# Kernel optimization log

Measured on AMD Instinct MI355X. Metric: run time of the kernel, lower is better.

Reference implementation:

```python
import jax, jax.numpy as jnp
import numpy as np

DIM = 192
HEADS = 6
HIDDEN = 384  # int(DIM * 2.0)


def _ln(x, w, b):
    # WithBias LayerNorm over channel dim (torch normalizes last dim of b,(hw),c)
    mu = jnp.mean(x, axis=1, keepdims=True)
    var = jnp.var(x, axis=1, keepdims=True)
    return (x - mu) / jnp.sqrt(var + 1e-5) * w[None, :, None, None] + b[None, :, None, None]


def _conv1x1(x, w):  # w: [O, I, 1, 1]
    return jnp.einsum('bihw,oi->bohw', x, w[:, :, 0, 0])


def _dwconv3(x, w):  # depthwise 3x3, w: [C, 1, 3, 3]
    return jax.lax.conv_general_dilated(
        x, w, window_strides=(1, 1), padding=((1, 1), (1, 1)),
        feature_group_count=x.shape[1],
        dimension_numbers=('NCHW', 'OIHW', 'NCHW'))


def _l2norm(x):  # F.normalize along last axis
    n = jnp.sqrt(jnp.sum(x * x, axis=-1, keepdims=True))
    return x / jnp.maximum(n, 1e-12)


def setup_inputs() -> dict:
    key = jax.random.key(0)
    ks = jax.random.split(key, 16)
    s = 0.02
    d = {}
    d['x'] = jax.random.normal(ks[0], (2, DIM, 128, 128), dtype=jnp.float32)
    d['k_v'] = jax.random.normal(ks[1], (2, 256), dtype=jnp.float32)
    d['ln1_w'] = jnp.ones((DIM,), jnp.float32)
    d['ln1_b'] = jnp.zeros((DIM,), jnp.float32)
    d['temp'] = jnp.ones((HEADS, 1, 1), jnp.float32)
    d['w_kR'] = jax.random.normal(ks[2], (DIM * 3 // 4, 192), jnp.float32) * s
    d['w_kI'] = jax.random.normal(ks[3], (DIM // 4, 64), jnp.float32) * s
    d['w_qR'] = jax.random.normal(ks[4], (DIM, DIM * 3 // 4, 1, 1), jnp.float32) * s
    d['w_qdw'] = jax.random.normal(ks[5], (DIM, 1, 3, 3), jnp.float32) * s
    d['w_kvI'] = jax.random.normal(ks[6], (DIM * 2, DIM // 4, 1, 1), jnp.float32) * s
    d['w_kvdw'] = jax.random.normal(ks[7], (DIM * 2, 1, 3, 3), jnp.float32) * s
    d['w_po'] = jax.random.normal(ks[8], (DIM, DIM, 1, 1), jnp.float32) * s
    d['ln2_w'] = jnp.ones((DIM,), jnp.float32)
    d['ln2_b'] = jnp.zeros((DIM,), jnp.float32)
    d['w_ffk'] = jax.random.normal(ks[9], (DIM, 256), jnp.float32) * s
    d['w_pin'] = jax.random.normal(ks[10], (HIDDEN * 2, DIM, 1, 1), jnp.float32) * s
    d['w_dw'] = jax.random.normal(ks[11], (HIDDEN * 2, 1, 3, 3), jnp.float32) * s
    d['w_pout'] = jax.random.normal(ks[12], (DIM, HIDDEN, 1, 1), jnp.float32) * s
    return d


def reference(x, k_v, ln1_w, ln1_b, temp, w_kR, w_kI, w_qR, w_qdw, w_kvI, w_kvdw,
              w_po, ln2_w, ln2_b, w_ffk, w_pin, w_dw, w_pout):
    b, c, h, w = x.shape
    c3 = c * 3 // 4
    # ---- Rttention on norm1(x) ----
    xn = _ln(x, ln1_w, ln1_b)
    kvr = (k_v[:, :192] @ w_kR.T)[:, :, None, None]   # [b, 3c/4, 1, 1]
    kvi = (k_v[:, 192:] @ w_kI.T)[:, :, None, None]   # [b, c/4, 1, 1]
    x_r = xn[:, :c3] * kvr + xn[:, :c3]
    x_i = xn[:, c3:] * kvi + xn[:, c3:]
    q = _dwconv3(_conv1x1(x_r, w_qR), w_qdw)          # [b, c, h, w]
    kv = _dwconv3(_conv1x1(x_i, w_kvI), w_kvdw)       # [b, 2c, h, w]
    k, v = jnp.split(kv, 2, axis=1)
    rh = lambda t: t.reshape(b, HEADS, c // HEADS, h * w)
    q = _l2norm(rh(q))
    k = _l2norm(rh(k))
    v = rh(v)
    # channel-wise attention: [b, head, c_h, c_h]
    attn = jax.nn.softmax(jnp.einsum('bhcd,bhed->bhce', q, k) * temp[None], axis=-1)
    out = jnp.einsum('bhce,bhed->bhcd', attn, v).reshape(b, c, h, w)
    x = x + _conv1x1(out, w_po)
    # ---- GDFN FeedForward on norm2(x) ----
    xn2 = _ln(x, ln2_w, ln2_b)
    kvf = (k_v @ w_ffk.T)[:, :, None, None]           # [b, c, 1, 1]
    y = xn2 * kvf + xn2
    y = _dwconv3(_conv1x1(y, w_pin), w_dw)            # [b, 2*hidden, h, w]
    y1, y2 = jnp.split(y, 2, axis=1)
    y = jax.nn.gelu(y1, approximate=False) * y2
    x = x + _conv1x1(y, w_pout)
    return (x, k_v)
```

## Files before the change

### kernel.cpp

```cpp
#include <hip/hip_runtime.h>
#include <math.h>

#define HW 16384
#define CDIM 192
#define C3 144
#define C4 48
#define NB 2
#define NPX 32768
#define HEADS 6

typedef unsigned short u16;
typedef unsigned int u32;
typedef __attribute__((ext_vector_type(8))) short bf16x8;
typedef __attribute__((ext_vector_type(4))) float f32x4;

__device__ __forceinline__ float bf2f(u16 u) {
    return __uint_as_float(((unsigned int)u) << 16);
}
__device__ __forceinline__ u16 f2bf(float f) {
    unsigned int x = __float_as_uint(f);
    unsigned int r = x + 0x7fffu + ((x >> 16) & 1u);
    return (u16)(r >> 16);
}

static inline float* wsf(void* ws, size_t off) { return (float*)((char*)ws + off); }
static inline u16* wsh(void* ws, size_t off) { return (u16*)((char*)ws + off); }

__global__ void k_setup(const float* __restrict__ kvv, const float* __restrict__ wkR,
                        const float* __restrict__ wkI, const float* __restrict__ wffk,
                        const float* __restrict__ wqR, const float* __restrict__ wkvI,
                        const float* __restrict__ wpo, const float* __restrict__ wpin,
                        const float* __restrict__ wpout,
                        const float* __restrict__ ln2w, const float* __restrict__ ln2b,
                        u16* __restrict__ wb, float* __restrict__ sm,
                        float* __restrict__ A2, float* __restrict__ B2,
                        float* __restrict__ tail) {
    int t = blockIdx.x * 256 + threadIdx.x;
    if (t < 313344) {
        float v;
        if (t < 30720) {
            int o = t / 160, i = t % 160;
            v = (i < 144) ? wqR[o * 144 + i] : 0.f;
        } else if (t < 55296) {
            int r = t - 30720; int o = r / 64, i = r % 64;
            v = (i < 48) ? wkvI[o * 48 + i] : 0.f;
        } else if (t < 92160) {
            v = wpo[t - 55296];
        } else if (t < 239616) {
            v = wpin[t - 92160];
        } else {
            v = wpout[t - 239616];
        }
        wb[t] = f2bf(v);
    } else if (t < 314112) {
        int r = t - 313344;
        if (r < 288) {
            int b = r / 144, o = r % 144;
            const float* v = kvv + b * 256;
            const float* w = wkR + o * 192;
            float s = 0.f;
            for (int j = 0; j < 192; j++) s += v[j] * w[j];
            sm[r] = s + 1.0f;
        } else if (r < 384) {
            int r2 = r - 288;
            int b = r2 / 48, o = r2 % 48;
            const float* v = kvv + b * 256 + 192;
            const float* w = wkI + o * 64;
            float s = 0.f;
            for (int j = 0; j < 64; j++) s += v[j] * w[j];
            sm[288 + r2] = s + 1.0f;
        } else {
            int r2 = r - 384;
            int b = r2 / 192, o = r2 % 192;
            const float* v = kvv + b * 256;
            const float* w = wffk + o * 256;
            float s = 0.f;
            for (int j = 0; j < 256; j++) s += v[j] * w[j];
            float sc = s + 1.0f;
            sm[384 + r2] = sc;
            A2[r2] = ln2w[o] * sc;
            B2[r2] = ln2b[o] * sc;
        }
    } else if (t < 314624) {
        int r = t - 314112;
        tail[r] = kvv[r];
    }
}

__global__ __launch_bounds__(256) void k_ln1(
    const float* __restrict__ xin,
    const float* __restrict__ lnw, const float* __restrict__ lnb,
    const float* __restrict__ sca, const float* __restrict__ scb,
    u16* __restrict__ outA, u16* __restrict__ outB) {
    __shared__ float red[2][16][16][4];
    __shared__ float mu_s[16][4], rstd_s[16][4];
    int t = threadIdx.x;
    int px4 = t & 15, cg = t >> 4;
    int base = blockIdx.x * 64;
    int b = base >> 14;
    int p = (base & 16383) + px4 * 4;
    float vals[12][4];
    float s[4] = {0.f, 0.f, 0.f, 0.f}, s2[4] = {0.f, 0.f, 0.f, 0.f};
#pragma unroll
    for (int j = 0; j < 12; j++) {
        int c = cg * 12 + j;
        size_t off = ((size_t)(b * CDIM + c)) * HW + p;
        float4 f = *(const float4*)(xin + off);
        float v[4] = {f.x, f.y, f.z, f.w};
#pragma unroll
        for (int q = 0; q < 4; q++) {
            vals[j][q] = v[q]; s[q] += v[q]; s2[q] += v[q] * v[q];
        }
    }
#pragma unroll
    for (int q = 0; q < 4; q++) { red[0][cg][px4][q] = s[q]; red[1][cg][px4][q] = s2[q]; }
    __syncthreads();
    if (t < 16) {
        float S[4] = {0.f, 0.f, 0.f, 0.f}, S2[4] = {0.f, 0.f, 0.f, 0.f};
        for (int g2 = 0; g2 < 16; g2++)
#pragma unroll
            for (int q = 0; q < 4; q++) { S[q] += red[0][g2][t][q]; S2[q] += red[1][g2][t][q]; }
#pragma unroll
        for (int q = 0; q < 4; q++) {
            float mu = S[q] * (1.0f / CDIM);
            float var = S2[q] * (1.0f / CDIM) - mu * mu;
            mu_s[t][q] = mu;
            rstd_s[t][q] = rsqrtf(var + 1e-5f);
        }
    }
    __syncthreads();
    float mu[4], rs[4];
#pragma unroll
    for (int q = 0; q < 4; q++) { mu[q] = mu_s[px4][q]; rs[q] = rstd_s[px4][q]; }
    float Ac[12], Bc[12];
#pragma unroll
    for (int j = 0; j < 12; j++) {
        int c = cg * 12 + j;
        float sc = (c < C3) ? sca[b * C3 + c] : scb[b * C4 + (c - C3)];
        Ac[j] = lnw[c] * sc;
        Bc[j] = lnb[c] * sc;
    }
    int isR = (cg < 12);
    size_t row0 = (size_t)b * HW + p;
    u16* basep = isR ? (outA + row0 * 160 + cg * 12)
                     : (outB + row0 * 64 + (cg * 12 - 144));
    int rowlen = isR ? 160 : 64;
#pragma unroll
    for (int q = 0; q < 4; q++) {
        u16 tmp[12];
#pragma unroll
        for (int j = 0; j < 12; j++)
            tmp[j] = f2bf((vals[j][q] - mu[q]) * rs[q] * Ac[j] + Bc[j]);
        u16* op = basep + q * rowlen;
        ushort4 o0 = {tmp[0], tmp[1], tmp[2], tmp[3]};
        ushort4 o1 = {tmp[4], tmp[5], tmp[6], tmp[7]};
        ushort4 o2 = {tmp[8], tmp[9], tmp[10], tmp[11]};
        *(ushort4*)(op) = o0;
        *(ushort4*)(op + 4) = o1;
        *(ushort4*)(op + 8) = o2;
    }
    if (cg == 0) {
        int4 z = {0, 0, 0, 0};
#pragma unroll
        for (int q = 0; q < 4; q++) {
            u16* pr = outA + (row0 + q) * 160 + 144;
            *(int4*)(pr) = z; *(int4*)(pr + 8) = z;
            u16* pi = outB + (row0 + q) * 64 + 48;
            *(int4*)(pi) = z; *(int4*)(pi + 8) = z;
        }
    }
}

template <int NCH, int MODE>
__global__ __launch_bounds__(256) void k_gemm_t(
    const u16* __restrict__ X, const u16* __restrict__ Wb,
    const void* __restrict__ resid, void* __restrict__ outp, int CO) {
    constexpr int CIP = NCH * 32;
    __shared__ __align__(16) u16 Xs[128 * 40];
    __shared__ __align__(16) u16 Wsh[64 * 40];
    const int tid = threadIdx.x;
    const int n0 = blockIdx.x * 128;
    const int m0 = blockIdx.y * 64;
    const int b = blockIdx.z;
    const int wave = tid >> 6, lane = tid & 63;
    const int quad = lane >> 4, l16 = lane & 15;
    const int spx = tid >> 1, sh = tid & 1;
    const int swr = tid >> 2, swc = tid & 3;
    const u16* xsrc = X + ((size_t)b * HW + n0 + spx) * CIP + sh * 16;
    const u16* wsrc = Wb + (size_t)(m0 + swr) * CIP + swc * 8;
    int4 xr0 = *(const int4*)(xsrc);
    int4 xr1 = *(const int4*)(xsrc + 8);
    int4 wr0 = *(const int4*)(wsrc);
    f32x4 acc[4][2] = {};
#pragma unroll
    for (int ch = 0; ch < NCH; ch++) {
        if (ch) __syncthreads();
        *(int4*)&Xs[spx * 40 + sh * 16] = xr0;
        *(int4*)&Xs[spx * 40 + sh * 16 + 8] = xr1;
        *(int4*)&Wsh[swr * 40 + swc * 8] = wr0;
        if (ch + 1 < NCH) {
            xr0 = *(const int4*)(xsrc + (ch + 1) * 32);
            xr1 = *(const int4*)(xsrc + (ch + 1) * 32 + 8);
            wr0 = *(const int4*)(wsrc + (ch + 1) * 32);
        }
        __syncthreads();
        bf16x8 af[4];
#pragma unroll
        for (int mi = 0; mi < 4; mi++)
            af[mi] = *(const bf16x8*)&Wsh[(mi * 16 + l16) * 40 + quad * 8];
        bf16x8 bf0 = *(const bf16x8*)&Xs[(wave * 32 + l16) * 40 + quad * 8];
        bf16x8 bf1 = *(const bf16x8*)&Xs[(wave * 32 + 16 + l16) * 40 + quad * 8];
#pragma unroll
        for (int mi = 0; mi < 4; mi++) {
            acc[mi][0] = __builtin_amdgcn_mfma_f32_16x16x32_bf16(af[mi], bf0, acc[mi][0], 0, 0, 0);
            acc[mi][1] = __builtin_amdgcn_mfma_f32_16x16x32_bf16(af[mi], bf1, acc[mi][1], 0, 0, 0);
        }
    }
#pragma unroll
    for (int mi = 0; mi < 4; mi++) {
#pragma unroll
        for (int ni = 0; ni < 2; ni++) {
            int c0 = m0 + mi * 16 + quad * 4;
            int px = n0 + wave * 32 + ni * 16 + l16;
            if (MODE == 0) {
                u16* ob = (u16*)outp + ((size_t)b * CO + c0) * HW + px;
#pragma unroll
                for (int rr = 0; rr < 4; rr++) ob[(size_t)rr * HW] = f2bf(acc[mi][ni][rr]);
            } else {
                const float* rp = (const float*)resid + ((size_t)b * 192 + c0) * HW + px;
                ushort4 o;
                o.x = f2bf(acc[mi][ni][0] + rp[0]);
                o.y = f2bf(acc[mi][ni][1] + rp[(size_t)HW]);
                o.z = f2bf(acc[mi][ni][2] + rp[(size_t)2 * HW]);
                o.w = f2bf(acc[mi][ni][3] + rp[(size_t)3 * HW]);
                *(ushort4*)((u16*)outp + ((size_t)b * HW + px) * 192 + c0) = o;
            }
        }
    }
}

__global__ __launch_bounds__(256) void k_gemm_s(
    const u16* __restrict__ X, const u16* __restrict__ Wb,
    const u16* __restrict__ residT, float* __restrict__ outp) {
    constexpr int NCH = 12;
    constexpr int CIP = NCH * 32;
    __shared__ __align__(16) u16 Ws[64 * 32];
    __shared__ __align__(16) u16 Xs[32 * 130];
    const int tid = threadIdx.x;
    const int n0 = blockIdx.x * 128;
    const int m0 = blockIdx.y * 64;
    const int b = blockIdx.z;
    const u16* Xb = X + (size_t)b * 384 * HW + n0;
    const int wave = tid >> 6, lane = tid & 63;
    const int quad = lane >> 4, l16 = lane & 15;
    const int smr = tid >> 2, sk4 = tid & 3;
    const int skr = tid >> 3, sc0 = (tid & 7) * 16;
    f32x4 acc[4][2] = {};
    for (int ch = 0; ch < NCH; ch++) {
        const int k0 = ch * 32;
        if (ch) __syncthreads();
        {
            const int4 wv = *(const int4*)(Wb + (size_t)(m0 + smr) * CIP + k0 + sk4 * 8);
            *(int4*)&Ws[(smr << 5) + (((sk4 ^ (smr & 3)) & 3) << 3)] = wv;
        }
        {
            const u16* xc = Xb + (size_t)(k0 + skr) * HW + sc0;
            int4 r0 = *(const int4*)xc;
            int4 r1 = *(const int4*)(xc + 8);
            u32* dst = (u32*)&Xs[skr * 130 + sc0];
#pragma unroll
            for (int i = 0; i < 4; i++) dst[i] = ((const u32*)&r0)[i];
#pragma unroll
            for (int i = 0; i < 4; i++) dst[4 + i] = ((const u32*)&r1)[i];
        }
        __syncthreads();
        bf16x8 af[4];
#pragma unroll
        for (int mi = 0; mi < 4; mi++) {
            int row = mi * 16 + l16;
            af[mi] = *(const bf16x8*)&Ws[(row << 5) + ((quad ^ (row & 3)) << 3)];
        }
#pragma unroll
        for (int ni = 0; ni < 2; ni++) {
            int n = wave * 32 + ni * 16 + l16;
            bf16x8 bfr;
#pragma unroll
            for (int j = 0; j < 8; j++) bfr[j] = (short)Xs[(quad * 8 + j) * 130 + n];
#pragma unroll
            for (int mi = 0; mi < 4; mi++)
                acc[mi][ni] = __builtin_amdgcn_mfma_f32_16x16x32_bf16(af[mi], bfr, acc[mi][ni], 0, 0, 0);
        }
    }
#pragma unroll
    for (int mi = 0; mi < 4; mi++) {
#pragma unroll
        for (int ni = 0; ni < 2; ni++) {
            int c0 = m0 + mi * 16 + quad * 4;
            int px = n0 + wave * 32 + ni * 16 + l16;
            ushort4 rv = *(const ushort4*)(residT + ((size_t)b * HW + px) * 192 + c0);
            float* ob = outp + ((size_t)b * 192 + c0) * HW + px;
            ob[0] = acc[mi][ni][0] + bf2f(rv.x);
            ob[(size_t)HW] = acc[mi][ni][1] + bf2f(rv.y);
            ob[(size_t)2 * HW] = acc[mi][ni][2] + bf2f(rv.z);
            ob[(size_t)3 * HW] = acc[mi][ni][3] + bf2f(rv.w);
        }
    }
}

__global__ __launch_bounds__(256) void k_dw2(const u16* __restrict__ X,
                                             const float* __restrict__ Wd,
                                             u16* __restrict__ out, int C, int sqCh,
                                             float* __restrict__ sqp) {
    __shared__ float In[34 * 132];
    __shared__ float red[4];
    int bc = blockIdx.x >> 2, rt = blockIdx.x & 3;
    int b = bc / C, ch = bc % C;
    const u16* xb = X + (size_t)bc * HW;
    int t = threadIdx.x;
    int c0 = (t & 7) * 16;
    for (int r = t >> 3; r < 34; r += 32) {
        int y = rt * 32 - 1 + r;
        float* dst = &In[r * 132 + 1 + c0];
        if ((unsigned)y < 128u) {
            const u16* src = xb + y * 128 + c0;
            int4 r0 = *(const int4*)src;
            int4 r1 = *(const int4*)(src + 8);
            const u16* p0 = (const u16*)&r0;
            const u16* p1 = (const u16*)&r1;
#pragma unroll
            for (int i = 0; i < 8; i++) dst[i] = bf2f(p0[i]);
#pragma unroll
            for (int i = 0; i < 8; i++) dst[8 + i] = bf2f(p1[i]);
        } else {
#pragma unroll
            for (int i = 0; i < 16; i++) dst[i] = 0.f;
        }
    }
    if (t < 34) { In[t * 132] = 0.f; In[t * 132 + 129] = 0.f; }
    __syncthreads();
    const float* w = Wd + ch * 9;
    float w00 = w[0], w01 = w[1], w02 = w[2], w10 = w[3], w11 = w[4],
          w12 = w[5], w20 = w[6], w21 = w[7], w22 = w[8];
    int x = t & 127, rg = t >> 7;
    int base = rg * 16;
    float A2 = 0.f, A1 = 0.f, B1 = 0.f, ssq = 0.f;
    u16* ob = out + (size_t)bc * HW + (rt * 32 + base) * 128 + x;
#pragma unroll
    for (int r = 0; r < 18; r++) {
        const float* row = &In[(base + r) * 132 + x];
        float v0 = row[0], v1 = row[1], v2 = row[2];
        float h0 = w00 * v0 + w01 * v1 + w02 * v2;
        float h1 = w10 * v0 + w11 * v1 + w12 * v2;
        float h2 = w20 * v0 + w21 * v1 + w22 * v2;
        if (r >= 2) {
            float val = A2 + B1 + h2;
            ob[(size_t)(r - 2) * 128] = f2bf(val);
            ssq += val * val;
        }
        A2 = A1; A1 = h0; B1 = h1;
    }
    if (ch < sqCh) {
        for (int o = 32; o > 0; o >>= 1) ssq += __shfl_down(ssq, o, 64);
        int wid = t >> 6, lane = t & 63;
        if (lane == 0) red[wid] = ssq;
        __syncthreads();
        if (t == 0) sqp[((b * 192 + ch) << 2) | rt] = red[0] + red[1] + red[2] + red[3];
    }
}

__global__ __launch_bounds__(256) void k_dw_gelu2(const u16* __restrict__ G0,
                                                  const float* __restrict__ Wd,
                                                  u16* __restrict__ out) {
    __shared__ float In[2 * 34 * 132];
    int bc = blockIdx.x >> 2, rt = blockIdx.x & 3;
    int b = bc / 384, j = bc % 384;
    int t = threadIdx.x;
    int c0 = (t & 7) * 16;
    for (int pl = 0; pl < 2; pl++) {
        const u16* xb = G0 + ((size_t)b * 768 + pl * 384 + j) * HW;
        float* pla = &In[pl * 34 * 132];
        for (int r = t >> 3; r < 34; r += 32) {
            int y = rt * 32 - 1 + r;
            float* dst = &pla[r * 132 + 1 + c0];
            if ((unsigned)y < 128u) {
                const u16* src = xb + y * 128 + c0;
                int4 r0 = *(const int4*)src;
                int4 r1 = *(const int4*)(src + 8);
                const u16* p0 = (const u16*)&r0;
                const u16* p1 = (const u16*)&r1;
#pragma unroll
                for (int i = 0; i < 8; i++) dst[i] = bf2f(p0[i]);
#pragma unroll
                for (int i = 0; i < 8; i++) dst[8 + i] = bf2f(p1[i]);
            } else {
#pragma unroll
                for (int i = 0; i < 16; i++) dst[i] = 0.f;
            }
        }
        if (t < 34) { pla[t * 132] = 0.f; pla[t * 132 + 129] = 0.f; }
    }
    __syncthreads();
    const float* w1 = Wd + j * 9;
    const float* w2 = Wd + (384 + j) * 9;
    float a00 = w1[0], a01 = w1[1], a02 = w1[2], a10 = w1[3], a11 = w1[4],
          a12 = w1[5], a20 = w1[6], a21 = w1[7], a22 = w1[8];
    float b00 = w2[0], b01 = w2[1], b02 = w2[2], b10 = w2[3], b11 = w2[4],
          b12 = w2[5], b20 = w2[6], b21 = w2[7], b22 = w2[8];
    int x = t & 127, rg = t >> 7;
    int base = rg * 16;
    float A2a = 0.f, A1a = 0.f, B1a = 0.f;
    float A2b = 0.f, A1b = 0.f, B1b = 0.f;
    u16* ob = out + ((size_t)b * 384 + j) * HW + (rt * 32 + base) * 128 + x;
#pragma unroll
    for (int r = 0; r < 18; r++) {
        const float* r1p = &In[(base + r) * 132 + x];
        const float* r2p = r1p + 34 * 132;
        float u0 = r1p[0], u1 = r1p[1], u2 = r1p[2];
        float v0 = r2p[0], v1 = r2p[1], v2 = r2p[2];
        float h0a = a00 * u0 + a01 * u1 + a02 * u2;
        float h1a = a10 * u0 + a11 * u1 + a12 * u2;
        float h2a = a20 * u0 + a21 * u1 + a22 * u2;
        float h0b = b00 * v0 + b01 * v1 + b02 * v2;
        float h1b = b10 * v0 + b11 * v1 + b12 * v2;
        float h2b = b20 * v0 + b21 * v1 + b22 * v2;
        if (r >= 2) {
            float s1 = A2a + B1a + h2a;
            float s2 = A2b + B1b + h2b;
            float g = 0.5f * s1 * (1.0f + erff(s1 * 0.70710678118654752f));
            ob[(size_t)(r - 2) * 128] = f2bf(g * s2);
        }
        A2a = A1a; A1a = h0a; B1a = h1a;
        A2b = A1b; A1b = h0b; B1b = h1b;
    }
}

__global__ __launch_bounds__(256) void k_qk(const u16* __restrict__ qb_,
                                            const u16* __restrict__ kb_,
                                            float* __restrict__ Spart) {
    int bh = blockIdx.x >> 6, ds = blockIdx.x & 63;
    int b = bh / HEADS, h = bh % HEADS;
    int tid = threadIdx.x;
    int wave = tid >> 6, lane = tid & 63;
    int quad = lane >> 4, l16 = lane & 15;
    int tm = wave >> 1, tn = wave & 1;
    const u16* qrow = qb_ + ((size_t)(b * 192 + h * 32 + tm * 16 + l16)) * HW + ds * 256 + quad * 8;
    const u16* krow = kb_ + ((size_t)(b * 384 + h * 32 + tn * 16 + l16)) * HW + ds * 256 + quad * 8;
    f32x4 acc = {};
    bf16x8 qa[3], ka[3];
    auto ld = [&](int s, int cc) {
        qa[s] = *(const bf16x8*)(qrow + cc * 32);
        ka[s] = *(const bf16x8*)(krow + cc * 32);
    };
    ld(0, 0); ld(1, 1);
#pragma unroll
    for (int ch = 0; ch < 8; ch++) {
        if (ch + 2 < 8) ld((ch + 2) % 3, ch + 2);
        acc = __builtin_amdgcn_mfma_f32_16x16x32_bf16(qa[ch % 3], ka[ch % 3], acc, 0, 0, 0);
    }
    float* Sb = Spart + ((size_t)ds * 12 + bh) * 1024;
#pragma unroll
    for (int r = 0; r < 4; r++)
        Sb[(tm * 16 + quad * 4 + r) * 32 + tn * 16 + l16] = acc[r];
}

__global__ void k_softmax(const float* __restrict__ Spart, const float* __restrict__ sqqp,
                          const float* __restrict__ sqkp, const float* __restrict__ temp,
                          u16* __restrict__ attnb) {
    int row = blockIdx.x;
    int bh = row >> 5, c2 = row & 31;
    int b = bh / HEADS, h = bh % HEADS;
    int e = threadIdx.x;
    float l = -1e30f;
    if (e < 32) {
        float s = 0.f;
        for (int d = 0; d < 64; d++) s += Spart[((size_t)d * 12 + bh) * 1024 + c2 * 32 + e];
        const float* qp = sqqp + (b * 192 + h * 32 + c2) * 4;
        const float* kp = sqkp + (b * 192 + h * 32 + e) * 4;
        float nq = qp[0] + qp[1] + qp[2] + qp[3];
        float nk = kp[0] + kp[1] + kp[2] + kp[3];
        float invq = 1.0f / fmaxf(sqrtf(nq), 1e-12f);
        float invk = 1.0f / fmaxf(sqrtf(nk), 1e-12f);
        l = s * invq * invk * temp[h];
    }
    float m = l;
    for (int o = 32; o > 0; o >>= 1) m = fmaxf(m, __shfl_xor(m, o, 64));
    float ev = (e < 32) ? expf(l - m) : 0.f;
    float ssum = ev;
    for (int o = 32; o > 0; o >>= 1) ssum += __shfl_xor(ssum, o, 64);
    if (e < 32) attnb[bh * 1024 + c2 * 32 + e] = f2bf(ev / ssum);
}

__global__ __launch_bounds__(256) void k_av(const u16* __restrict__ attnb,
                                            const u16* __restrict__ kvb,
                                            u16* __restrict__ out) {
    __shared__ __align__(16) u16 Vs[32 * 130];
    int bh = blockIdx.x >> 7;
    int pt = blockIdx.x & 127;
    int b = bh / HEADS, h = bh % HEADS;
    int p0 = pt * 128;
    int t = threadIdx.x;
    {
        int e = t >> 3, c0 = (t & 7) * 16;
        const u16* src = kvb + ((size_t)(b * 384 + 192 + h * 32 + e)) * HW + p0 + c0;
        int4 r0 = *(const int4*)src;
        int4 r1 = *(const int4*)(src + 8);
        u32* dst = (u32*)&Vs[e * 130 + c0];
#pragma unroll
        for (int i = 0; i < 4; i++) dst[i] = ((const u32*)&r0)[i];
#pragma unroll
        for (int i = 0; i < 4; i++) dst[4 + i] = ((const u32*)&r1)[i];
    }
    __syncthreads();
    int wave = t >> 6, lane = t & 63;
    int quad = lane >> 4, l16 = lane & 15;
    f32x4 acc[2][2] = {};
    bf16x8 af[2];
#pragma unroll
    for (int tm = 0; tm < 2; tm++)
        af[tm] = *(const bf16x8*)(attnb + bh * 1024 + (tm * 16 + l16) * 32 + quad * 8);
#pragma unroll
    for (int nt = 0; nt < 2; nt++) {
        int n = wave * 32 + nt * 16 + l16;
        bf16x8 bfr;
#pragma unroll
        for (int j = 0; j < 8; j++) bfr[j] = (short)Vs[(quad * 8 + j) * 130 + n];
#pragma unroll
        for (int tm = 0; tm < 2; tm++)
            acc[tm][nt] = __builtin_amdgcn_mfma_f32_16x16x32_bf16(af[tm], bfr, acc[tm][nt], 0, 0, 0);
    }
#pragma unroll
    for (int tm = 0; tm < 2; tm++)
#pragma unroll
        for (int nt = 0; nt < 2; nt++) {
            int c0 = h * 32 + tm * 16 + quad * 4;
            int px = p0 + wave * 32 + nt * 16 + l16;
            ushort4 o;
            o.x = f2bf(acc[tm][nt][0]);
            o.y = f2bf(acc[tm][nt][1]);
            o.z = f2bf(acc[tm][nt][2]);
            o.w = f2bf(acc[tm][nt][3]);
            *(ushort4*)(out + ((size_t)b * HW + px) * 192 + c0) = o;
        }
}

__global__ __launch_bounds__(256) void k_ln2t(
    const u16* __restrict__ xin, const float* __restrict__ A2,
    const float* __restrict__ B2, u16* __restrict__ outp) {
    int t = threadIdx.x;
    int pxg = blockIdx.x * 64 + (t >> 2);
    int l2 = t & 3;
    int b = pxg >> 14;
    const u16* src = xin + (size_t)pxg * 192 + l2 * 48;
    float v[48];
    float s = 0.f, s2 = 0.f;
#pragma unroll
    for (int i = 0; i < 6; i++) {
        int4 r0 = *(const int4*)(src + i * 8);
        const u16* pp = (const u16*)&r0;
#pragma unroll
        for (int k = 0; k < 8; k++) {
            float f = bf2f(pp[k]);
            v[i * 8 + k] = f; s += f; s2 += f * f;
        }
    }
    s += __shfl_xor(s, 1, 64);  s += __shfl_xor(s, 2, 64);
    s2 += __shfl_xor(s2, 1, 64); s2 += __shfl_xor(s2, 2, 64);
    float mu = s * (1.0f / CDIM);
    float rstd = rsqrtf(s2 * (1.0f / CDIM) - mu * mu + 1e-5f);
    const float* Ap = A2 + b * 192 + l2 * 48;
    const float* Bp = B2 + b * 192 + l2 * 48;
    u16* dst = outp + (size_t)pxg * 192 + l2 * 48;
#pragma unroll
    for (int i = 0; i < 12; i++) {
        float4 a = *(const float4*)(Ap + i * 4);
        float4 bb = *(const float4*)(Bp + i * 4);
        ushort4 o;
        o.x = f2bf((v[i * 4 + 0] - mu) * rstd * a.x + bb.x);
        o.y = f2bf((v[i * 4 + 1] - mu) * rstd * a.y + bb.y);
        o.z = f2bf((v[i * 4 + 2] - mu) * rstd * a.z + bb.z);
        o.w = f2bf((v[i * 4 + 3] - mu) * rstd * a.w + bb.w);
        *(ushort4*)(dst + i * 4) = o;
    }
}

extern "C" void kernel_launch(void* const* d_in, const int* in_sizes, int n_in,
                              void* d_out, int out_size, void* d_ws, size_t ws_size,
                              hipStream_t stream) {
    const float* x     = (const float*)d_in[0];
    const float* k_v   = (const float*)d_in[1];
    const float* ln1w  = (const float*)d_in[2];
    const float* ln1b  = (const float*)d_in[3];
    const float* temp  = (const float*)d_in[4];
    const float* w_kR  = (const float*)d_in[5];
    const float* w_kI  = (const float*)d_in[6];
    const float* w_qR  = (const float*)d_in[7];
    const float* w_qdw = (const float*)d_in[8];
    const float* w_kvI = (const float*)d_in[9];
    const float* w_kvdw= (const float*)d_in[10];
    const float* w_po  = (const float*)d_in[11];
    const float* ln2w  = (const float*)d_in[12];
    const float* ln2b  = (const float*)d_in[13];
    const float* w_ffk = (const float*)d_in[14];
    const float* w_pin = (const float*)d_in[15];
    const float* w_dw  = (const float*)d_in[16];
    const float* w_pout= (const float*)d_in[17];
    float* out = (float*)d_out;

    const size_t MiB = 1048576ULL;
    u16*   q0b     = wsh(d_ws, 0);
    u16*   attnoutb= wsh(d_ws, 0);
    u16*   y0b     = wsh(d_ws, 0);
    u16*   kv0b    = wsh(d_ws, 12 * MiB);
    u16*   ybufb   = wsh(d_ws, 12 * MiB);
    u16*   x1b     = wsh(d_ws, 36 * MiB);
    u16*   qbuf_b  = wsh(d_ws, 48 * MiB);
    u16*   kvbuf_b = wsh(d_ws, 60 * MiB);
    u16*   xrb     = wsh(d_ws, 84 * MiB);
    u16*   xib     = wsh(d_ws, 94 * MiB);
    u16*   g0b     = wsh(d_ws, 98 * MiB);
    u16*   wb      = wsh(d_ws, 146 * MiB);
    float* sm      = wsf(d_ws, 147 * MiB);
    float* Spart   = wsf(d_ws, 0);
    u16* wq   = wb;
    u16* wkv  = wb + 30720;
    u16* wpo  = wb + 55296;
    u16* wpin = wb + 92160;
    u16* wpout= wb + 239616;
    float* kvr  = sm;
    float* kvi  = sm + 288;
    float* sqqp = sm + 768;
    float* sqkp = sm + 2304;
    u16*   attnb= (u16*)(sm + 3840);
    float* A2c  = sm + 10240;
    float* B2c  = sm + 10624;

    k_setup<<<1229, 256, 0, stream>>>(k_v, w_kR, w_kI, w_ffk, w_qR, w_kvI, w_po,
                                      w_pin, w_pout, ln2w, ln2b, wb, sm, A2c, B2c,
                                      out + (size_t)NB * CDIM * HW);
    k_ln1<<<NPX / 64, 256, 0, stream>>>(x, ln1w, ln1b, kvr, kvi, xrb, xib);
    k_gemm_t<5, 0><<<dim3(128, 3, 2), 256, 0, stream>>>(xrb, wq, nullptr, q0b, 192);
    k_gemm_t<2, 0><<<dim3(128, 6, 2), 256, 0, stream>>>(xib, wkv, nullptr, kv0b, 384);
    k_dw2<<<NB * 192 * 4, 256, 0, stream>>>(q0b, w_qdw, qbuf_b, 192, 192, sqqp);
    k_dw2<<<NB * 384 * 4, 256, 0, stream>>>(kv0b, w_kvdw, kvbuf_b, 384, 192, sqkp);
    k_qk<<<12 * 64, 256, 0, stream>>>(qbuf_b, kvbuf_b, Spart);
    k_softmax<<<384, 64, 0, stream>>>(Spart, sqqp, sqkp, temp, attnb);
    k_av<<<12 * 128, 256, 0, stream>>>(attnb, kvbuf_b, attnoutb);
    k_gemm_t<6, 1><<<dim3(128, 3, 2), 256, 0, stream>>>(attnoutb, wpo, x, x1b, 192);
    k_ln2t<<<NPX / 64, 256, 0, stream>>>(x1b, A2c, B2c, y0b);
    k_gemm_t<6, 0><<<dim3(128, 12, 2), 256, 0, stream>>>(y0b, wpin, nullptr, g0b, 768);
    k_dw_gelu2<<<NB * 384 * 4, 256, 0, stream>>>(g0b, w_dw, ybufb);
    k_gemm_s<<<dim3(128, 3, 2), 256, 0, stream>>>(ybufb, wpout, x1b, out);
}
```

Baseline: 262.4 us.

## Fuse output projection GEMM with residual and LayerNorm2; vectorize depthwise smem staging

Adds a new GEMM kernel for the attention output projection in which each block computes all 192 output channels for 64 pixels. This lets it add the residual and apply LayerNorm2 with the k_v scale in registers, writing both x1 and the normalized FFN input, so the separate LN2 pass and its reread of x1 go away. The depthwise-conv kernels pad shared-memory rows to 136 floats so bf16 inputs can be staged with float4 stores, and the setup dot-product loops get unroll pragmas. In exchange, the fused kernel holds 12 accumulators plus a 48-float array per thread, which may raise register pressure, and it reads the residual with a strided per-channel pattern.

```diff
diff --git a/kernel.cpp b/kernel.cpp
--- a/kernel.cpp
+++ b/kernel.cpp
@@ -59,6 +59,7 @@
             const float* v = kvv + b * 256;
             const float* w = wkR + o * 192;
             float s = 0.f;
+#pragma unroll 8
             for (int j = 0; j < 192; j++) s += v[j] * w[j];
             sm[r] = s + 1.0f;
         } else if (r < 384) {
@@ -67,6 +68,7 @@
             const float* v = kvv + b * 256 + 192;
             const float* w = wkI + o * 64;
             float s = 0.f;
+#pragma unroll 8
             for (int j = 0; j < 64; j++) s += v[j] * w[j];
             sm[288 + r2] = s + 1.0f;
         } else {
@@ -75,6 +77,7 @@
             const float* v = kvv + b * 256;
             const float* w = wffk + o * 256;
             float s = 0.f;
+#pragma unroll 8
             for (int j = 0; j < 256; j++) s += v[j] * w[j];
             float sc = s + 1.0f;
             sm[384 + r2] = sc;
@@ -236,6 +239,83 @@
                 *(ushort4*)((u16*)outp + ((size_t)b * HW + px) * 192 + c0) = o;
             }
         }
+    }
+}
+
+__global__ __launch_bounds__(256) void k_gemm_po(
+    const u16* __restrict__ X, const u16* __restrict__ Wb,
+    const float* __restrict__ resid, const float* __restrict__ A2,
+    const float* __restrict__ B2, u16* __restrict__ x1T, u16* __restrict__ y0T) {
+    constexpr int CIP = 192;
+    __shared__ __align__(16) u16 Xs[64 * 40];
+    __shared__ __align__(16) u16 Wsh[192 * 40];
+    const int tid = threadIdx.x;
+    const int n0 = blockIdx.x * 64;
+    const int b = blockIdx.y;
+    const int wave = tid >> 6, lane = tid & 63;
+    const int quad = lane >> 4, l16 = lane & 15;
+    const int spx = tid >> 2, sk = tid & 3;
+    const u16* xsrc = X + ((size_t)b * HW + n0 + spx) * CIP + sk * 8;
+    const u16* wsrc = Wb + (size_t)spx * CIP + sk * 8;
+    int4 xr = *(const int4*)xsrc;
+    int4 w0 = *(const int4*)(wsrc);
+    int4 w1 = *(const int4*)(wsrc + 64 * CIP);
+    int4 w2 = *(const int4*)(wsrc + 128 * CIP);
+    f32x4 acc[12] = {};
+#pragma unroll
+    for (int ch = 0; ch < 6; ch++) {
+        if (ch) __syncthreads();
+        *(int4*)&Xs[spx * 40 + sk * 8] = xr;
+        *(int4*)&Wsh[spx * 40 + sk * 8] = w0;
+        *(int4*)&Wsh[(spx + 64) * 40 + sk * 8] = w1;
+        *(int4*)&Wsh[(spx + 128) * 40 + sk * 8] = w2;
+        if (ch + 1 < 6) {
+            xr = *(const int4*)(xsrc + (ch + 1) * 32);
+            w0 = *(const int4*)(wsrc + (ch + 1) * 32);
+            w1 = *(const int4*)(wsrc + 64 * CIP + (ch + 1) * 32);
+            w2 = *(const int4*)(wsrc + 128 * CIP + (ch + 1) * 32);
+        }
+        __syncthreads();
+        bf16x8 bf = *(const bf16x8*)&Xs[(wave * 16 + l16) * 40 + quad * 8];
+#pragma unroll
+        for (int mi = 0; mi < 12; mi++) {
+            bf16x8 af = *(const bf16x8*)&Wsh[(mi * 16 + l16) * 40 + quad * 8];
+            acc[mi] = __builtin_amdgcn_mfma_f32_16x16x32_bf16(af, bf, acc[mi], 0, 0, 0);
+        }
+    }
+    int px = n0 + wave * 16 + l16;
+    float v[48];
+    float s = 0.f, s2 = 0.f;
+    const float* rb = resid + (size_t)b * 192 * HW + px;
+#pragma unroll
+    for (int mi = 0; mi < 12; mi++) {
+        int c0 = mi * 16 + quad * 4;
+#pragma unroll
+        for (int r = 0; r < 4; r++) {
+            float val = acc[mi][r] + rb[(size_t)(c0 + r) * HW];
+            v[mi * 4 + r] = val; s += val; s2 += val * val;
+        }
+    }
+    s += __shfl_xor(s, 16, 64);  s += __shfl_xor(s, 32, 64);
+    s2 += __shfl_xor(s2, 16, 64); s2 += __shfl_xor(s2, 32, 64);
+    float mu = s * (1.0f / CDIM);
+    float rstd = rsqrtf(s2 * (1.0f / CDIM) - mu * mu + 1e-5f);
+    u16* xd = x1T + ((size_t)b * HW + px) * 192;
+    u16* yd = y0T + ((size_t)b * HW + px) * 192;
+#pragma unroll
+    for (int mi = 0; mi < 12; mi++) {
+        int c0 = mi * 16 + quad * 4;
+        float4 a4 = *(const float4*)(A2 + b * 192 + c0);
+        float4 b4 = *(const float4*)(B2 + b * 192 + c0);
+        ushort4 xo, yo;
+        xo.x = f2bf(v[mi * 4 + 0]); xo.y = f2bf(v[mi * 4 + 1]);
+        xo.z = f2bf(v[mi * 4 + 2]); xo.w = f2bf(v[mi * 4 + 3]);
+        yo.x = f2bf((v[mi * 4 + 0] - mu) * rstd * a4.x + b4.x);
+        yo.y = f2bf((v[mi * 4 + 1] - mu) * rstd * a4.y + b4.y);
+        yo.z = f2bf((v[mi * 4 + 2] - mu) * rstd * a4.z + b4.z);
+        yo.w = f2bf((v[mi * 4 + 3] - mu) * rstd * a4.w + b4.w);
+        *(ushort4*)(xd + c0) = xo;
+        *(ushort4*)(yd + c0) = yo;
     }
 }
 
@@ -311,7 +391,7 @@
                                              const float* __restrict__ Wd,
                                              u16* __restrict__ out, int C, int sqCh,
                                              float* __restrict__ sqp) {
-    __shared__ float In[34 * 132];
+    __shared__ float In[34 * 136];
     __shared__ float red[4];
     int bc = blockIdx.x >> 2, rt = blockIdx.x & 3;
     int b = bc / C, ch = bc % C;
@@ -320,23 +400,26 @@
     int c0 = (t & 7) * 16;
     for (int r = t >> 3; r < 34; r += 32) {
         int y = rt * 32 - 1 + r;
-        float* dst = &In[r * 132 + 1 + c0];
+        float* dst = &In[r * 136 + 4 + c0];
         if ((unsigned)y < 128u) {
             const u16* src = xb + y * 128 + c0;
             int4 r0 = *(const int4*)src;
             int4 r1 = *(const int4*)(src + 8);
             const u16* p0 = (const u16*)&r0;
             const u16* p1 = (const u16*)&r1;
-#pragma unroll
-            for (int i = 0; i < 8; i++) dst[i] = bf2f(p0[i]);
-#pragma unroll
-            for (int i = 0; i < 8; i++) dst[8 + i] = bf2f(p1[i]);
+            float4 f0 = {bf2f(p0[0]), bf2f(p0[1]), bf2f(p0[2]), bf2f(p0[3])};
+            float4 f1 = {bf2f(p0[4]), bf2f(p0[5]), bf2f(p0[6]), bf2f(p0[7])};
+            float4 f2 = {bf2f(p1[0]), bf2f(p1[1]), bf2f(p1[2]), bf2f(p1[3])};
+            float4 f3 = {bf2f(p1[4]), bf2f(p1[5]), bf2f(p1[6]), bf2f(p1[7])};
+            *(float4*)(dst) = f0;      *(float4*)(dst + 4) = f1;
+            *(float4*)(dst + 8) = f2;  *(float4*)(dst + 12) = f3;
         } else {
-#pragma unroll
-            for (int i = 0; i < 16; i++) dst[i] = 0.f;
-        }
-    }
-    if (t < 34) { In[t * 132] = 0.f; In[t * 132 + 129] = 0.f; }
+            float4 z = {0.f, 0.f, 0.f, 0.f};
+            *(float4*)(dst) = z;      *(float4*)(dst + 4) = z;
+            *(float4*)(dst + 8) = z;  *(float4*)(dst + 12) = z;
+        }
+    }
+    if (t < 34) { In[t * 136 + 3] = 0.f; In[t * 136 + 132] = 0.f; }
     __syncthreads();
     const float* w = Wd + ch * 9;
     float w00 = w[0], w01 = w[1], w02 = w[2], w10 = w[3], w11 = w[4],
@@ -347,7 +430,7 @@
     u16* ob = out + (size_t)bc * HW + (rt * 32 + base) * 128 + x;
 #pragma unroll
     for (int r = 0; r < 18; r++) {
-        const float* row = &In[(base + r) * 132 + x];
+        const float* row = &In[(base + r) * 136 + 3 + x];
         float v0 = row[0], v1 = row[1], v2 = row[2];
         float h0 = w00 * v0 + w01 * v1 + w02 * v2;
         float h1 = w10 * v0 + w11 * v1 + w12 * v2;
@@ -371,33 +454,36 @@
 __global__ __launch_bounds__(256) void k_dw_gelu2(const u16* __restrict__ G0,
                                                   const float* __restrict__ Wd,
                                                   u16* __restrict__ out) {
-    __shared__ float In[2 * 34 * 132];
+    __shared__ float In[2 * 34 * 136];
     int bc = blockIdx.x >> 2, rt = blockIdx.x & 3;
     int b = bc / 384, j = bc % 384;
     int t = threadIdx.x;
     int c0 = (t & 7) * 16;
     for (int pl = 0; pl < 2; pl++) {
         const u16* xb = G0 + ((size_t)b * 768 + pl * 384 + j) * HW;
-        float* pla = &In[pl * 34 * 132];
+        float* pla = &In[pl * 34 * 136];
         for (int r = t >> 3; r < 34; r += 32) {
             int y = rt * 32 - 1 + r;
-            float* dst = &pla[r * 132 + 1 + c0];
+            float* dst = &pla[r * 136 + 4 + c0];
             if ((unsigned)y < 128u) {
                 const u16* src = xb + y * 128 + c0;
                 int4 r0 = *(const int4*)src;
                 int4 r1 = *(const int4*)(src + 8);
                 const u16* p0 = (const u16*)&r0;
                 const u16* p1 = (const u16*)&r1;
-#pragma unroll
-                for (int i = 0; i < 8; i++) dst[i] = bf2f(p0[i]);
-#pragma unroll
-                for (int i = 0; i < 8; i++) dst[8 + i] = bf2f(p1[i]);
+                float4 f0 = {bf2f(p0[0]), bf2f(p0[1]), bf2f(p0[2]), bf2f(p0[3])};
+                float4 f1 = {bf2f(p0[4]), bf2f(p0[5]), bf2f(p0[6]), bf2f(p0[7])};
+                float4 f2 = {bf2f(p1[0]), bf2f(p1[1]), bf2f(p1[2]), bf2f(p1[3])};
+                float4 f3 = {bf2f(p1[4]), bf2f(p1[5]), bf2f(p1[6]), bf2f(p1[7])};
+                *(float4*)(dst) = f0;      *(float4*)(dst + 4) = f1;
+                *(float4*)(dst + 8) = f2;  *(float4*)(dst + 12) = f3;
             } else {
-#pragma unroll
-                for (int i = 0; i < 16; i++) dst[i] = 0.f;
+                float4 z = {0.f, 0.f, 0.f, 0.f};
+                *(float4*)(dst) = z;      *(float4*)(dst + 4) = z;
+                *(float4*)(dst + 8) = z;  *(float4*)(dst + 12) = z;
             }
         }
-        if (t < 34) { pla[t * 132] = 0.f; pla[t * 132 + 129] = 0.f; }
+        if (t < 34) { pla[t * 136 + 3] = 0.f; pla[t * 136 + 132] = 0.f; }
     }
     __syncthreads();
     const float* w1 = Wd + j * 9;
@@ -413,8 +499,8 @@
     u16* ob = out + ((size_t)b * 384 + j) * HW + (rt * 32 + base) * 128 + x;
 #pragma unroll
     for (int r = 0; r < 18; r++) {
-        const float* r1p = &In[(base + r) * 132 + x];
-        const float* r2p = r1p + 34 * 132;
+        const float* r1p = &In[(base + r) * 136 + 3 + x];
+        const float* r2p = r1p + 34 * 136;
         float u0 = r1p[0], u1 = r1p[1], u2 = r1p[2];
         float v0 = r2p[0], v1 = r2p[1], v2 = r2p[2];
         float h0a = a00 * u0 + a01 * u1 + a02 * u2;
@@ -541,46 +627,6 @@
             o.w = f2bf(acc[tm][nt][3]);
             *(ushort4*)(out + ((size_t)b * HW + px) * 192 + c0) = o;
         }
-}
-
-__global__ __launch_bounds__(256) void k_ln2t(
-    const u16* __restrict__ xin, const float* __restrict__ A2,
-    const float* __restrict__ B2, u16* __restrict__ outp) {
-    int t = threadIdx.x;
-    int pxg = blockIdx.x * 64 + (t >> 2);
-    int l2 = t & 3;
-    int b = pxg >> 14;
-    const u16* src = xin + (size_t)pxg * 192 + l2 * 48;
-    float v[48];
-    float s = 0.f, s2 = 0.f;
-#pragma unroll
-    for (int i = 0; i < 6; i++) {
-        int4 r0 = *(const int4*)(src + i * 8);
-        const u16* pp = (const u16*)&r0;
-#pragma unroll
-        for (int k = 0; k < 8; k++) {
-            float f = bf2f(pp[k]);
-            v[i * 8 + k] = f; s += f; s2 += f * f;
-        }
-    }
-    s += __shfl_xor(s, 1, 64);  s += __shfl_xor(s, 2, 64);
-    s2 += __shfl_xor(s2, 1, 64); s2 += __shfl_xor(s2, 2, 64);
-    float mu = s * (1.0f / CDIM);
-    float rstd = rsqrtf(s2 * (1.0f / CDIM) - mu * mu + 1e-5f);
-    const float* Ap = A2 + b * 192 + l2 * 48;
-    const float* Bp = B2 + b * 192 + l2 * 48;
-    u16* dst = outp + (size_t)pxg * 192 + l2 * 48;
-#pragma unroll
-    for (int i = 0; i < 12; i++) {
-        float4 a = *(const float4*)(Ap + i * 4);
-        float4 bb = *(const float4*)(Bp + i * 4);
-        ushort4 o;
-        o.x = f2bf((v[i * 4 + 0] - mu) * rstd * a.x + bb.x);
-        o.y = f2bf((v[i * 4 + 1] - mu) * rstd * a.y + bb.y);
-        o.z = f2bf((v[i * 4 + 2] - mu) * rstd * a.z + bb.z);
-        o.w = f2bf((v[i * 4 + 3] - mu) * rstd * a.w + bb.w);
-        *(ushort4*)(dst + i * 4) = o;
-    }
 }
 
 extern "C" void kernel_launch(void* const* d_in, const int* in_sizes, int n_in,
@@ -645,8 +691,7 @@
     k_qk<<<12 * 64, 256, 0, stream>>>(qbuf_b, kvbuf_b, Spart);
     k_softmax<<<384, 64, 0, stream>>>(Spart, sqqp, sqkp, temp, attnb);
     k_av<<<12 * 128, 256, 0, stream>>>(attnb, kvbuf_b, attnoutb);
-    k_gemm_t<6, 1><<<dim3(128, 3, 2), 256, 0, stream>>>(attnoutb, wpo, x, x1b, 192);
-    k_ln2t<<<NPX / 64, 256, 0, stream>>>(x1b, A2c, B2c, y0b);
+    k_gemm_po<<<dim3(256, 2), 256, 0, stream>>>(attnoutb, wpo, x, A2c, B2c, x1b, y0b);
     k_gemm_t<6, 0><<<dim3(128, 12, 2), 256, 0, stream>>>(y0b, wpin, nullptr, g0b, 768);
     k_dw_gelu2<<<NB * 384 * 4, 256, 0, stream>>>(g0b, w_dw, ybufb);
     k_gemm_s<<<dim3(128, 3, 2), 256, 0, stream>>>(ybufb, wpout, x1b, out);
```

Result: no change. 258.0 us (-1.7%).
